# Optimization experiments

Hardware: AMD Instinct MI355X
Metric: run time of the kernel (lower is better)

## Reference

```python
import jax, jax.numpy as jnp
import numpy as np

N = 131072          # total packed nodes
NODES = 256         # nodes per graph (equal, contiguous segments)
D = 128             # input_dim


def setup_inputs() -> dict:
    key = jax.random.key(0)
    k_x, k_q, k_k, k_v, k_bq, k_bk, k_bv = jax.random.split(key, 7)
    lim = 1.0 / np.sqrt(D)  # nn.Linear default init range
    return {
        "x": jax.random.normal(k_x, (N, D), dtype=jnp.float32),
        # contiguous equal-size graph ids: 512 graphs of 256 nodes
        "batch": (jnp.arange(N) // NODES).astype(jnp.int64),
        "Wq": jax.random.uniform(k_q, (D, D), jnp.float32, -lim, lim),
        "bq": jax.random.uniform(k_bq, (D,), jnp.float32, -lim, lim),
        "Wk": jax.random.uniform(k_k, (D, D), jnp.float32, -lim, lim),
        "bk": jax.random.uniform(k_bk, (D,), jnp.float32, -lim, lim),
        "Wv": jax.random.uniform(k_v, (D, D), jnp.float32, -lim, lim),
        "bv": jax.random.uniform(k_bv, (D,), jnp.float32, -lim, lim),
    }


def reference(x, batch, Wq, bq, Wk, bk, Wv, bv):
    # batch holds contiguous equal-size segments (built in setup_inputs),
    # so the per-graph Python loop of the original collapses to one batched
    # block-diagonal attention: reshape [N, D] -> [B, n, D].
    n, d = NODES, x.shape[-1]
    xb = x.reshape(-1, n, d)                      # [B, n, d]
    q = xb @ Wq.T + bq                            # nn.Linear: x W^T + b
    k = xb @ Wk.T + bk
    v = xb @ Wv.T + bv
    scale = jnp.sqrt(jnp.asarray(d, dtype=x.dtype))
    scores = jnp.einsum("bnd,bmd->bnm", q, k) / scale   # [B, n, n]
    w = jax.nn.softmax(scores, axis=-1)
    out = jnp.einsum("bnm,bmd->bnd", w, v)
    return out.reshape(x.shape)
```

## Files before the change

### kernel.cpp

```cpp
#include <hip/hip_runtime.h>


typedef float f32x4 __attribute__((ext_vector_type(4)));
typedef unsigned int u32x2 __attribute__((ext_vector_type(2)));
typedef unsigned int u32x4 __attribute__((ext_vector_type(4)));
typedef short s16x4 __attribute__((ext_vector_type(4)));

#define SCALE 0.088388347648318447f

__device__ __forceinline__ unsigned bf16pk(float a, float b) {
    unsigned ua = __builtin_bit_cast(unsigned, a);
    unsigned ub = __builtin_bit_cast(unsigned, b);
    ua += 0x7fffu + ((ua >> 16) & 1u);
    ub += 0x7fffu + ((ub >> 16) & 1u);
    return (ua >> 16) | (ub & 0xffff0000u);
}

__device__ __forceinline__ unsigned short bf16s(float a) {
    unsigned ua = __builtin_bit_cast(unsigned, a);
    ua += 0x7fffu + ((ua >> 16) & 1u);
    return (unsigned short)(ua >> 16);
}

__device__ __forceinline__ f32x4 mfma16(u32x2 a, u32x2 b, f32x4 c) {
    return __builtin_amdgcn_mfma_f32_16x16x16bf16_1k(
        __builtin_bit_cast(s16x4, a), __builtin_bit_cast(s16x4, b), c, 0, 0, 0);
}

__device__ __forceinline__ int ks_off(int row, int d) {
    return ((row << 8) + (d << 1)) ^ ((row & 7) << 4);
}
__device__ __forceinline__ int vt_off(int j, int k) {
    return (65536 + (j << 9) + (k << 1)) ^ ((j & 7) << 3);
}
__device__ __forceinline__ int w_off(int j, int d) {
    return (65536 + (j << 8) + (d << 1)) ^ ((j & 7) << 4);
}

extern "C" __global__ void __launch_bounds__(512, 2)
sattn(const float* __restrict__ x,
      const float* __restrict__ Wq, const float* __restrict__ bq,
      const float* __restrict__ Wk, const float* __restrict__ bk,
      const float* __restrict__ Wv, const float* __restrict__ bv,
      float* __restrict__ out)
{
    extern __shared__ char sm[];
    const int t    = threadIdx.x;
    const int lane = t & 63;
    const int w    = t >> 6;
    const int h    = lane & 15;
    const int g    = lane >> 4;
    const int R0   = blockIdx.x << 8;
    const int wr0  = w << 5;

    u32x2 xf[2][8];
#pragma unroll
    for (int rt = 0; rt < 2; ++rt) {
        const float* xr = x + (size_t)(R0 + wr0 + 16 * rt + h) * 128 + 4 * g;
#pragma unroll
        for (int c = 0; c < 8; ++c) {
            f32x4 v = *(const f32x4*)(xr + 16 * c);
            xf[rt][c] = (u32x2){ bf16pk(v.x, v.y), bf16pk(v.z, v.w) };
        }
    }

    auto stageW = [&](const float* W) {
        const int j  = t >> 2;
        const int d0 = (t & 3) << 5;
        const float* src = W + j * 128 + d0;
#pragma unroll
        for (int m2 = 0; m2 < 4; ++m2) {
            f32x4 a = *(const f32x4*)(src + 8 * m2);
            f32x4 b = *(const f32x4*)(src + 8 * m2 + 4);
            u32x4 p = (u32x4){ bf16pk(a.x, a.y), bf16pk(a.z, a.w),
                               bf16pk(b.x, b.y), bf16pk(b.z, b.w) };
            *(u32x4*)(sm + w_off(j, d0 + 8 * m2)) = p;
        }
    };

    stageW(Wq);
    __syncthreads();
    u32x2 qf[8][2];
#pragma unroll
    for (int jt = 0; jt < 8; ++jt) {
        f32x4 b4 = *(const f32x4*)(bq + 16 * jt + 4 * g);
        f32x4 a0 = b4, a1 = b4;
#pragma unroll
        for (int c = 0; c < 8; ++c) {
            u32x2 wf = *(const u32x2*)(sm + w_off(h + 16 * jt, 16 * c + 4 * g));
            a0 = mfma16(wf, xf[0][c], a0);
            a1 = mfma16(wf, xf[1][c], a1);
        }
        qf[jt][0] = (u32x2){ bf16pk(a0.x * SCALE, a0.y * SCALE), bf16pk(a0.z * SCALE, a0.w * SCALE) };
        qf[jt][1] = (u32x2){ bf16pk(a1.x * SCALE, a1.y * SCALE), bf16pk(a1.z * SCALE, a1.w * SCALE) };
    }
    __syncthreads();

    stageW(Wk);
    __syncthreads();
#pragma unroll
    for (int jt = 0; jt < 8; ++jt) {
        float bkj = bk[h + 16 * jt];
        f32x4 a0 = { bkj, bkj, bkj, bkj }, a1 = a0;
#pragma unroll
        for (int c = 0; c < 8; ++c) {
            u32x2 wf = *(const u32x2*)(sm + w_off(h + 16 * jt, 16 * c + 4 * g));
            a0 = mfma16(xf[0][c], wf, a0);
            a1 = mfma16(xf[1][c], wf, a1);
        }
#pragma unroll
        for (int r = 0; r < 4; ++r) {
            *(unsigned short*)(sm + ks_off(wr0 + 4 * g + r,      h + 16 * jt)) = bf16s(a0[r]);
            *(unsigned short*)(sm + ks_off(wr0 + 16 + 4 * g + r, h + 16 * jt)) = bf16s(a1[r]);
        }
    }
    __syncthreads();

    stageW(Wv);
    __syncthreads();
    u32x2 vpk[2][8];
#pragma unroll
    for (int jt = 0; jt < 8; ++jt) {
        float bvj = bv[h + 16 * jt];
        f32x4 a0 = { bvj, bvj, bvj, bvj }, a1 = a0;
#pragma unroll
        for (int c = 0; c < 8; ++c) {
            u32x2 wf = *(const u32x2*)(sm + w_off(h + 16 * jt, 16 * c + 4 * g));
            a0 = mfma16(xf[0][c], wf, a0);
            a1 = mfma16(xf[1][c], wf, a1);
        }
        vpk[0][jt] = (u32x2){ bf16pk(a0.x, a0.y), bf16pk(a0.z, a0.w) };
        vpk[1][jt] = (u32x2){ bf16pk(a1.x, a1.y), bf16pk(a1.z, a1.w) };
    }
    __syncthreads();
#pragma unroll
    for (int jt = 0; jt < 8; ++jt) {
        *(u32x2*)(sm + vt_off(h + 16 * jt, wr0 + 4 * g))      = vpk[0][jt];
        *(u32x2*)(sm + vt_off(h + 16 * jt, wr0 + 16 + 4 * g)) = vpk[1][jt];
    }
    __syncthreads();

    f32x4 O[2][8];
#pragma unroll
    for (int qt = 0; qt < 2; ++qt)
#pragma unroll
        for (int jt = 0; jt < 8; ++jt)
            O[qt][jt] = (f32x4){ 0.f, 0.f, 0.f, 0.f };
    float ls0 = 0.f, ls1 = 0.f;

    for (int kc = 0; kc < 16; ++kc) {
        u32x2 kfr[8];
#pragma unroll
        for (int jt = 0; jt < 8; ++jt)
            kfr[jt] = *(const u32x2*)(sm + ks_off(16 * kc + h, 16 * jt + 4 * g));
        f32x4 s0 = { 0.f, 0.f, 0.f, 0.f }, s1 = s0;
#pragma unroll
        for (int jt = 0; jt < 8; ++jt) {
            s0 = mfma16(kfr[jt], qf[jt][0], s0);
            s1 = mfma16(kfr[jt], qf[jt][1], s1);
        }
        float e0[4], e1[4];
#pragma unroll
        for (int r = 0; r < 4; ++r) { e0[r] = __expf(s0[r]); e1[r] = __expf(s1[r]); }
        ls0 += e0[0] + e0[1] + e0[2] + e0[3];
        ls1 += e1[0] + e1[1] + e1[2] + e1[3];
        u32x2 pa0 = (u32x2){ bf16pk(e0[0], e0[1]), bf16pk(e0[2], e0[3]) };
        u32x2 pa1 = (u32x2){ bf16pk(e1[0], e1[1]), bf16pk(e1[2], e1[3]) };
#pragma unroll
        for (int jt = 0; jt < 8; ++jt) {
            u32x2 vf = *(const u32x2*)(sm + vt_off(h + 16 * jt, 16 * kc + 4 * g));
            O[0][jt] = mfma16(pa0, vf, O[0][jt]);
            O[1][jt] = mfma16(pa1, vf, O[1][jt]);
        }
    }

    ls0 += __shfl_xor(ls0, 16); ls0 += __shfl_xor(ls0, 32);
    ls1 += __shfl_xor(ls1, 16); ls1 += __shfl_xor(ls1, 32);
    float li0 = 1.0f / ls0;
    float li1 = 1.0f / ls1;
#pragma unroll
    for (int r = 0; r < 4; ++r) {
        float ri0 = __shfl(li0, 4 * g + r);
        float ri1 = __shfl(li1, 4 * g + r);
        float* o0 = out + (size_t)(R0 + wr0 + 4 * g + r) * 128 + h;
        float* o1 = out + (size_t)(R0 + wr0 + 16 + 4 * g + r) * 128 + h;
#pragma unroll
        for (int jt = 0; jt < 8; ++jt) {
            o0[16 * jt] = O[0][jt][r] * ri0;
            o1[16 * jt] = O[1][jt][r] * ri1;
        }
    }
}

extern "C" void kernel_launch(void* const* d_in, const int* in_sizes, int n_in,
                              void* d_out, int out_size, void* d_ws, size_t ws_size,
                              hipStream_t stream) {
    const float* x  = (const float*)d_in[0];
    const float* Wq = (const float*)d_in[2];
    const float* bq = (const float*)d_in[3];
    const float* Wk = (const float*)d_in[4];
    const float* bk = (const float*)d_in[5];
    const float* Wv = (const float*)d_in[6];
    const float* bv = (const float*)d_in[7];
    float* out = (float*)d_out;

    hipFuncSetAttribute((const void*)sattn,
                        hipFuncAttributeMaxDynamicSharedMemorySize, 131072);
    sattn<<<dim3(512), dim3(512), 131072, stream>>>(x, Wq, bq, Wk, bk, Wv, bv, out);
}
```

Before: 82.65 us.

## Fold Wq·Wk into one matrix and apply Wv after attention

Scores are rewritten as x·(Wq^T Wk·scale)·x^T plus a per-key bias term, with the combined matrix and bias vector computed by a small pre-kernel into workspace. Keys become raw x in LDS instead of projected K. The value projection is moved after the attention sum (P·x then ·Wv^T plus bv), so V is never materialised. The main kernel also switches to 16x16x32 MFMA, uses an identity-MFMA to transpose operands, and cuts LDS so more blocks fit per CU. The cost is an extra launch and more rounding through bf16 intermediates.

```diff
diff --git a/kernel.cpp b/kernel.cpp
--- a/kernel.cpp
+++ b/kernel.cpp
@@ -5,8 +5,11 @@
 typedef unsigned int u32x2 __attribute__((ext_vector_type(2)));
 typedef unsigned int u32x4 __attribute__((ext_vector_type(4)));
 typedef short s16x4 __attribute__((ext_vector_type(4)));
+typedef short s16x8 __attribute__((ext_vector_type(8)));
 
 #define SCALE 0.088388347648318447f
+#define VOFF  65536
+#define LDSSZ 66560
 
 __device__ __forceinline__ unsigned bf16pk(float a, float b) {
     unsigned ua = __builtin_bit_cast(unsigned, a);
@@ -15,33 +18,52 @@
     ub += 0x7fffu + ((ub >> 16) & 1u);
     return (ua >> 16) | (ub & 0xffff0000u);
 }
-
 __device__ __forceinline__ unsigned short bf16s(float a) {
     unsigned ua = __builtin_bit_cast(unsigned, a);
     ua += 0x7fffu + ((ua >> 16) & 1u);
     return (unsigned short)(ua >> 16);
 }
-
 __device__ __forceinline__ f32x4 mfma16(u32x2 a, u32x2 b, f32x4 c) {
     return __builtin_amdgcn_mfma_f32_16x16x16bf16_1k(
         __builtin_bit_cast(s16x4, a), __builtin_bit_cast(s16x4, b), c, 0, 0, 0);
 }
+__device__ __forceinline__ f32x4 mfma32(u32x4 a, u32x4 b, f32x4 c) {
+    return __builtin_amdgcn_mfma_f32_16x16x32_bf16(
+        __builtin_bit_cast(s16x8, a), __builtin_bit_cast(s16x8, b), c, 0, 0, 0);
+}
 
 __device__ __forceinline__ int ks_off(int row, int d) {
-    return ((row << 8) + (d << 1)) ^ ((row & 7) << 4);
-}
-__device__ __forceinline__ int vt_off(int j, int k) {
-    return (65536 + (j << 9) + (k << 1)) ^ ((j & 7) << 3);
-}
-__device__ __forceinline__ int w_off(int j, int d) {
-    return (65536 + (j << 8) + (d << 1)) ^ ((j & 7) << 4);
-}
-
-extern "C" __global__ void __launch_bounds__(512, 2)
-sattn(const float* __restrict__ x,
-      const float* __restrict__ Wq, const float* __restrict__ bq,
-      const float* __restrict__ Wk, const float* __restrict__ bk,
-      const float* __restrict__ Wv, const float* __restrict__ bv,
+    return (row << 8) + (((d << 1)) ^ ((row & 15) << 3));
+}
+__device__ __forceinline__ int wf4_off(int j, int d) {
+    return (j << 8) + (((d << 1)) ^ ((j & 15) << 4));
+}
+
+extern "C" __global__ void __launch_bounds__(256)
+sattn_pre(const float* __restrict__ Wq, const float* __restrict__ bq,
+          const float* __restrict__ Wk, char* __restrict__ wsb)
+{
+    const int b = blockIdx.x, t = threadIdx.x;
+    if (b < 64) {
+        const int row = b * 2 + (t >> 7);
+        const int a   = t & 127;
+        float acc = 0.f;
+#pragma unroll 4
+        for (int o = 0; o < 128; ++o)
+            acc += Wq[o * 128 + a] * Wk[o * 128 + row];
+        *(unsigned short*)(wsb + wf4_off(row, a)) = bf16s(acc * SCALE);
+    } else if (t < 128) {
+        float acc = 0.f;
+#pragma unroll 4
+        for (int o = 0; o < 128; ++o)
+            acc += bq[o] * Wk[o * 128 + t];
+        *(float*)(wsb + 32768 + 4 * t) = acc * SCALE;
+    }
+}
+
+extern "C" __global__ void __launch_bounds__(512, 4)
+sattn(const float* __restrict__ x, const float* __restrict__ Wv,
+      const float* __restrict__ bv, const char* __restrict__ wsb,
       float* __restrict__ out)
 {
     extern __shared__ char sm[];
@@ -52,143 +74,176 @@
     const int g    = lane >> 4;
     const int R0   = blockIdx.x << 8;
     const int wr0  = w << 5;
+    const f32x4 Z  = {0.f, 0.f, 0.f, 0.f};
+
+    {
+        const u32x4* src = (const u32x4*)wsb;
+        u32x4* dst = (u32x4*)sm;
+#pragma unroll
+        for (int i = 0; i < 4; ++i) dst[t + 512 * i] = src[t + 512 * i];
+    }
 
     u32x2 xf[2][8];
+    float vp0 = 0.f, vp1 = 0.f;
+    const float* wvec = (const float*)(wsb + 32768);
 #pragma unroll
     for (int rt = 0; rt < 2; ++rt) {
         const float* xr = x + (size_t)(R0 + wr0 + 16 * rt + h) * 128 + 4 * g;
+        float vacc = 0.f;
 #pragma unroll
         for (int c = 0; c < 8; ++c) {
             f32x4 v = *(const f32x4*)(xr + 16 * c);
+            f32x4 wc = *(const f32x4*)(wvec + 16 * c + 4 * g);
+            vacc += v.x * wc.x + v.y * wc.y + v.z * wc.z + v.w * wc.w;
             xf[rt][c] = (u32x2){ bf16pk(v.x, v.y), bf16pk(v.z, v.w) };
         }
-    }
-
-    auto stageW = [&](const float* W) {
+        if (rt == 0) vp0 = vacc; else vp1 = vacc;
+    }
+    vp0 += __shfl_xor(vp0, 16); vp0 += __shfl_xor(vp0, 32);
+    vp1 += __shfl_xor(vp1, 16); vp1 += __shfl_xor(vp1, 32);
+    if (g == 0) {
+        *(float*)(sm + VOFF + (wr0 + h) * 4)      = vp0;
+        *(float*)(sm + VOFF + (wr0 + 16 + h) * 4) = vp1;
+    }
+    __syncthreads();
+
+    u32x2 yf[8][2];
+#pragma unroll
+    for (int jt = 0; jt < 8; ++jt) {
+        f32x4 a0 = Z, a1 = Z;
+#pragma unroll
+        for (int c2 = 0; c2 < 4; ++c2) {
+            u32x2 mlo = *(const u32x2*)(sm + wf4_off(h + 16 * jt, 32 * c2 + 4 * g));
+            u32x2 mhi = *(const u32x2*)(sm + wf4_off(h + 16 * jt, 32 * c2 + 16 + 4 * g));
+            u32x4 A = (u32x4){ mlo.x, mlo.y, mhi.x, mhi.y };
+            u32x4 B0 = (u32x4){ xf[0][2 * c2].x, xf[0][2 * c2].y, xf[0][2 * c2 + 1].x, xf[0][2 * c2 + 1].y };
+            u32x4 B1 = (u32x4){ xf[1][2 * c2].x, xf[1][2 * c2].y, xf[1][2 * c2 + 1].x, xf[1][2 * c2 + 1].y };
+            a0 = mfma32(A, B0, a0);
+            a1 = mfma32(A, B1, a1);
+        }
+        yf[jt][0] = (u32x2){ bf16pk(a0.x, a0.y), bf16pk(a0.z, a0.w) };
+        yf[jt][1] = (u32x2){ bf16pk(a1.x, a1.y), bf16pk(a1.z, a1.w) };
+    }
+    __syncthreads();
+
+#pragma unroll
+    for (int rt = 0; rt < 2; ++rt)
+#pragma unroll
+        for (int c = 0; c < 8; ++c)
+            *(u32x2*)(sm + ks_off(wr0 + 16 * rt + h, 16 * c + 4 * g)) = xf[rt][c];
+    __syncthreads();
+
+    const int ii = h - 4 * g;
+    u32x2 idf;
+    idf.x = (ii == 0 ? 0x3F80u : 0u) | (ii == 1 ? (0x3F80u << 16) : 0u);
+    idf.y = (ii == 2 ? 0x3F80u : 0u) | (ii == 3 ? (0x3F80u << 16) : 0u);
+
+    f32x4 Tacc[8][2];
+#pragma unroll
+    for (int jt = 0; jt < 8; ++jt) { Tacc[jt][0] = Z; Tacc[jt][1] = Z; }
+    float ls0 = 0.f, ls1 = 0.f;
+
+#pragma unroll 2
+    for (int kc2 = 0; kc2 < 8; ++kc2) {
+        u32x2 pe[2][2];
+#pragma unroll
+        for (int kk = 0; kk < 2; ++kk) {
+            const int kc = 2 * kc2 + kk;
+            f32x4 a0 = Z, a1 = Z;
+#pragma unroll
+            for (int c2 = 0; c2 < 4; ++c2) {
+                u32x2 xlo = *(const u32x2*)(sm + ks_off(16 * kc + h, 32 * c2 + 4 * g));
+                u32x2 xhi = *(const u32x2*)(sm + ks_off(16 * kc + h, 32 * c2 + 16 + 4 * g));
+                u32x4 A = (u32x4){ xlo.x, xlo.y, xhi.x, xhi.y };
+                u32x4 B0 = (u32x4){ yf[2 * c2][0].x, yf[2 * c2][0].y, yf[2 * c2 + 1][0].x, yf[2 * c2 + 1][0].y };
+                u32x4 B1 = (u32x4){ yf[2 * c2][1].x, yf[2 * c2][1].y, yf[2 * c2 + 1][1].x, yf[2 * c2 + 1][1].y };
+                a0 = mfma32(A, B0, a0);
+                a1 = mfma32(A, B1, a1);
+            }
+            f32x4 vv = *(const f32x4*)(sm + VOFF + (16 * kc + 4 * g) * 4);
+            float e0[4], e1[4];
+#pragma unroll
+            for (int r = 0; r < 4; ++r) {
+                e0[r] = __expf(a0[r] + vv[r]);
+                e1[r] = __expf(a1[r] + vv[r]);
+            }
+            ls0 += e0[0] + e0[1] + e0[2] + e0[3];
+            ls1 += e1[0] + e1[1] + e1[2] + e1[3];
+            pe[kk][0] = (u32x2){ bf16pk(e0[0], e0[1]), bf16pk(e0[2], e0[3]) };
+            pe[kk][1] = (u32x2){ bf16pk(e1[0], e1[1]), bf16pk(e1[2], e1[3]) };
+        }
+        u32x4 pa0 = (u32x4){ pe[0][0].x, pe[0][0].y, pe[1][0].x, pe[1][0].y };
+        u32x4 pa1 = (u32x4){ pe[0][1].x, pe[0][1].y, pe[1][1].x, pe[1][1].y };
+#pragma unroll
+        for (int jt = 0; jt < 8; ++jt) {
+            u32x2 ra = *(const u32x2*)(sm + ks_off(16 * (2 * kc2) + h,     16 * jt + 4 * g));
+            u32x2 rb = *(const u32x2*)(sm + ks_off(16 * (2 * kc2 + 1) + h, 16 * jt + 4 * g));
+            f32x4 ta = mfma16(ra, idf, Z);
+            f32x4 tb = mfma16(rb, idf, Z);
+            u32x4 tB = (u32x4){ bf16pk(ta.x, ta.y), bf16pk(ta.z, ta.w),
+                                bf16pk(tb.x, tb.y), bf16pk(tb.z, tb.w) };
+            Tacc[jt][0] = mfma32(pa0, tB, Tacc[jt][0]);
+            Tacc[jt][1] = mfma32(pa1, tB, Tacc[jt][1]);
+        }
+    }
+    __syncthreads();
+
+    {
         const int j  = t >> 2;
         const int d0 = (t & 3) << 5;
-        const float* src = W + j * 128 + d0;
+        const float* src = Wv + j * 128 + d0;
 #pragma unroll
         for (int m2 = 0; m2 < 4; ++m2) {
             f32x4 a = *(const f32x4*)(src + 8 * m2);
             f32x4 b = *(const f32x4*)(src + 8 * m2 + 4);
             u32x4 p = (u32x4){ bf16pk(a.x, a.y), bf16pk(a.z, a.w),
                                bf16pk(b.x, b.y), bf16pk(b.z, b.w) };
-            *(u32x4*)(sm + w_off(j, d0 + 8 * m2)) = p;
-        }
-    };
-
-    stageW(Wq);
-    __syncthreads();
-    u32x2 qf[8][2];
-#pragma unroll
-    for (int jt = 0; jt < 8; ++jt) {
-        f32x4 b4 = *(const f32x4*)(bq + 16 * jt + 4 * g);
-        f32x4 a0 = b4, a1 = b4;
-#pragma unroll
-        for (int c = 0; c < 8; ++c) {
-            u32x2 wf = *(const u32x2*)(sm + w_off(h + 16 * jt, 16 * c + 4 * g));
-            a0 = mfma16(wf, xf[0][c], a0);
-            a1 = mfma16(wf, xf[1][c], a1);
-        }
-        qf[jt][0] = (u32x2){ bf16pk(a0.x * SCALE, a0.y * SCALE), bf16pk(a0.z * SCALE, a0.w * SCALE) };
-        qf[jt][1] = (u32x2){ bf16pk(a1.x * SCALE, a1.y * SCALE), bf16pk(a1.z * SCALE, a1.w * SCALE) };
-    }
-    __syncthreads();
-
-    stageW(Wk);
-    __syncthreads();
-#pragma unroll
-    for (int jt = 0; jt < 8; ++jt) {
-        float bkj = bk[h + 16 * jt];
-        f32x4 a0 = { bkj, bkj, bkj, bkj }, a1 = a0;
-#pragma unroll
-        for (int c = 0; c < 8; ++c) {
-            u32x2 wf = *(const u32x2*)(sm + w_off(h + 16 * jt, 16 * c + 4 * g));
-            a0 = mfma16(xf[0][c], wf, a0);
-            a1 = mfma16(xf[1][c], wf, a1);
-        }
-#pragma unroll
-        for (int r = 0; r < 4; ++r) {
-            *(unsigned short*)(sm + ks_off(wr0 + 4 * g + r,      h + 16 * jt)) = bf16s(a0[r]);
-            *(unsigned short*)(sm + ks_off(wr0 + 16 + 4 * g + r, h + 16 * jt)) = bf16s(a1[r]);
-        }
-    }
-    __syncthreads();
-
-    stageW(Wv);
-    __syncthreads();
-    u32x2 vpk[2][8];
-#pragma unroll
-    for (int jt = 0; jt < 8; ++jt) {
-        float bvj = bv[h + 16 * jt];
-        f32x4 a0 = { bvj, bvj, bvj, bvj }, a1 = a0;
-#pragma unroll
-        for (int c = 0; c < 8; ++c) {
-            u32x2 wf = *(const u32x2*)(sm + w_off(h + 16 * jt, 16 * c + 4 * g));
-            a0 = mfma16(xf[0][c], wf, a0);
-            a1 = mfma16(xf[1][c], wf, a1);
-        }
-        vpk[0][jt] = (u32x2){ bf16pk(a0.x, a0.y), bf16pk(a0.z, a0.w) };
-        vpk[1][jt] = (u32x2){ bf16pk(a1.x, a1.y), bf16pk(a1.z, a1.w) };
-    }
-    __syncthreads();
-#pragma unroll
-    for (int jt = 0; jt < 8; ++jt) {
-        *(u32x2*)(sm + vt_off(h + 16 * jt, wr0 + 4 * g))      = vpk[0][jt];
-        *(u32x2*)(sm + vt_off(h + 16 * jt, wr0 + 16 + 4 * g)) = vpk[1][jt];
-    }
-    __syncthreads();
-
-    f32x4 O[2][8];
-#pragma unroll
-    for (int qt = 0; qt < 2; ++qt)
-#pragma unroll
-        for (int jt = 0; jt < 8; ++jt)
-            O[qt][jt] = (f32x4){ 0.f, 0.f, 0.f, 0.f };
-    float ls0 = 0.f, ls1 = 0.f;
-
-    for (int kc = 0; kc < 16; ++kc) {
-        u32x2 kfr[8];
-#pragma unroll
-        for (int jt = 0; jt < 8; ++jt)
-            kfr[jt] = *(const u32x2*)(sm + ks_off(16 * kc + h, 16 * jt + 4 * g));
-        f32x4 s0 = { 0.f, 0.f, 0.f, 0.f }, s1 = s0;
-#pragma unroll
-        for (int jt = 0; jt < 8; ++jt) {
-            s0 = mfma16(kfr[jt], qf[jt][0], s0);
-            s1 = mfma16(kfr[jt], qf[jt][1], s1);
-        }
-        float e0[4], e1[4];
-#pragma unroll
-        for (int r = 0; r < 4; ++r) { e0[r] = __expf(s0[r]); e1[r] = __expf(s1[r]); }
-        ls0 += e0[0] + e0[1] + e0[2] + e0[3];
-        ls1 += e1[0] + e1[1] + e1[2] + e1[3];
-        u32x2 pa0 = (u32x2){ bf16pk(e0[0], e0[1]), bf16pk(e0[2], e0[3]) };
-        u32x2 pa1 = (u32x2){ bf16pk(e1[0], e1[1]), bf16pk(e1[2], e1[3]) };
-#pragma unroll
-        for (int jt = 0; jt < 8; ++jt) {
-            u32x2 vf = *(const u32x2*)(sm + vt_off(h + 16 * jt, 16 * kc + 4 * g));
-            O[0][jt] = mfma16(pa0, vf, O[0][jt]);
-            O[1][jt] = mfma16(pa1, vf, O[1][jt]);
+            *(u32x4*)(sm + wf4_off(j, d0 + 8 * m2)) = p;
         }
     }
 
     ls0 += __shfl_xor(ls0, 16); ls0 += __shfl_xor(ls0, 32);
     ls1 += __shfl_xor(ls1, 16); ls1 += __shfl_xor(ls1, 32);
-    float li0 = 1.0f / ls0;
-    float li1 = 1.0f / ls1;
-#pragma unroll
-    for (int r = 0; r < 4; ++r) {
-        float ri0 = __shfl(li0, 4 * g + r);
-        float ri1 = __shfl(li1, 4 * g + r);
-        float* o0 = out + (size_t)(R0 + wr0 + 4 * g + r) * 128 + h;
-        float* o1 = out + (size_t)(R0 + wr0 + 16 + 4 * g + r) * 128 + h;
-#pragma unroll
-        for (int jt = 0; jt < 8; ++jt) {
-            o0[16 * jt] = O[0][jt][r] * ri0;
-            o1[16 * jt] = O[1][jt][r] * ri1;
-        }
+    const float li0 = 1.0f / ls0;
+    const float li1 = 1.0f / ls1;
+
+    u32x4 tBO[4][2];
+#pragma unroll
+    for (int c2 = 0; c2 < 4; ++c2) {
+#pragma unroll
+        for (int qt = 0; qt < 2; ++qt) {
+            f32x4 A0 = (qt == 0) ? Tacc[2 * c2][0]     : Tacc[2 * c2][1];
+            f32x4 A1 = (qt == 0) ? Tacc[2 * c2 + 1][0] : Tacc[2 * c2 + 1][1];
+            u32x2 p0 = (u32x2){ bf16pk(A0.x, A0.y), bf16pk(A0.z, A0.w) };
+            u32x2 p1 = (u32x2){ bf16pk(A1.x, A1.y), bf16pk(A1.z, A1.w) };
+            f32x4 d0 = mfma16(p0, idf, Z);
+            f32x4 d1 = mfma16(p1, idf, Z);
+            tBO[c2][qt] = (u32x4){ bf16pk(d0.x, d0.y), bf16pk(d0.z, d0.w),
+                                   bf16pk(d1.x, d1.y), bf16pk(d1.z, d1.w) };
+        }
+    }
+    __syncthreads();
+
+#pragma unroll
+    for (int ot = 0; ot < 8; ++ot) {
+        f32x4 o0 = Z, o1 = Z;
+#pragma unroll
+        for (int c2 = 0; c2 < 4; ++c2) {
+            u32x2 wlo = *(const u32x2*)(sm + wf4_off(h + 16 * ot, 32 * c2 + 4 * g));
+            u32x2 whi = *(const u32x2*)(sm + wf4_off(h + 16 * ot, 32 * c2 + 16 + 4 * g));
+            u32x4 A = (u32x4){ wlo.x, wlo.y, whi.x, whi.y };
+            o0 = mfma32(A, tBO[c2][0], o0);
+            o1 = mfma32(A, tBO[c2][1], o1);
+        }
+        f32x4 bvv = *(const f32x4*)(bv + 16 * ot + 4 * g);
+        f32x4 r0v, r1v;
+#pragma unroll
+        for (int r = 0; r < 4; ++r) {
+            r0v[r] = o0[r] * li0 + bvv[r];
+            r1v[r] = o1[r] * li1 + bvv[r];
+        }
+        *(f32x4*)(out + (size_t)(R0 + wr0 + h) * 128 + 16 * ot + 4 * g)      = r0v;
+        *(f32x4*)(out + (size_t)(R0 + wr0 + 16 + h) * 128 + 16 * ot + 4 * g) = r1v;
     }
 }
 
@@ -199,12 +254,14 @@
     const float* Wq = (const float*)d_in[2];
     const float* bq = (const float*)d_in[3];
     const float* Wk = (const float*)d_in[4];
-    const float* bk = (const float*)d_in[5];
     const float* Wv = (const float*)d_in[6];
     const float* bv = (const float*)d_in[7];
     float* out = (float*)d_out;
+    char* wsb = (char*)d_ws;
 
     hipFuncSetAttribute((const void*)sattn,
-                        hipFuncAttributeMaxDynamicSharedMemorySize, 131072);
-    sattn<<<dim3(512), dim3(512), 131072, stream>>>(x, Wq, bq, Wk, bk, Wv, bv, out);
-}
+                        hipFuncAttributeMaxDynamicSharedMemorySize, LDSSZ);
+
+    sattn_pre<<<dim3(65), dim3(256), 0, stream>>>(Wq, bq, Wk, wsb);
+    sattn<<<dim3(512), dim3(512), LDSSZ, stream>>>(x, Wv, bv, wsb, out);
+}
```

After: 177.5 us. 115% more time.
